# Kernel optimization log

Measured on AMD Instinct MI355X. Metric: run time of the kernel, lower is better.

## Reference

```python
import jax, jax.numpy as jnp
import numpy as np

B, S, D, E, H = 2, 1024, 1024, 16, 2048  # batch, seq, in_dim, num_experts, hidden_dim
TOP_K = 2
TEMP = 1.0


def setup_inputs() -> dict:
    key = jax.random.key(0)
    ks = jax.random.split(key, 4)
    sc_d = 1.0 / np.sqrt(D)
    sc_h = 1.0 / np.sqrt(H)
    return {
        "x": jax.random.normal(ks[0], (B, S, D), dtype=jnp.float32),
        "Wr": jax.random.normal(ks[1], (D, E), dtype=jnp.float32) * sc_d,  # router
        "br": jnp.zeros((E,), dtype=jnp.float32),
        "W1": jax.random.normal(ks[2], (E, D, H), dtype=jnp.float32) * sc_d,  # expert fc1
        "b1": jnp.zeros((E, H), dtype=jnp.float32),
        "W2": jax.random.normal(ks[3], (E, H, D), dtype=jnp.float32) * sc_h,  # expert fc2
        "b2": jnp.zeros((E, D), dtype=jnp.float32),
    }


def reference(x, Wr, br, W1, b1, W2, b2):
    token_shape = x.shape[:-1]
    d = x.shape[-1]
    xt = x.reshape(-1, d)  # [T, D] flattened tokens
    T = xt.shape[0]

    # Router: logits / temperature -> softmax -> top-k
    logits = (xt @ Wr + br) / TEMP
    probs = jax.nn.softmax(logits, axis=-1)          # [T, E]
    w, idx = jax.lax.top_k(probs, TOP_K)             # [T, K]
    w = w / jnp.clip(jnp.sum(w, axis=-1, keepdims=True), 1e-9)

    # Combine weights per (token, expert); top-k indices are unique per row
    comb = jnp.zeros((T, E), dtype=xt.dtype)
    comb = comb.at[jnp.arange(T)[:, None], idx].add(w)  # [T, E]

    # Per-expert 2-layer MLP with exact (erf) GELU, matching torch nn.GELU
    h = jax.nn.gelu(jnp.einsum('td,edh->teh', xt, W1) + b1, approximate=False)  # [T, E, H]
    o = jnp.einsum('teh,eho->teo', h, W2) + b2                                   # [T, E, D]
    y = jnp.einsum('teo,te->to', o, comb)                                        # [T, D]

    # residual (in_dim == out_dim)
    y = xt + y
    return y.reshape(*token_shape, d)
```

## Files before the change

kernel.cpp:

```cpp
#include <hip/hip_runtime.h>
#include <hip/hip_bf16.h>

#define T_TOK 2048
#define DIM   1024
#define NEXP  16
#define HID   2048
#define MAXMT 48

typedef __attribute__((ext_vector_type(8))) short short8;
typedef __attribute__((ext_vector_type(4))) float f32x4;

__device__ __forceinline__ unsigned short f2bf(float f) {
  __hip_bfloat16 h = __float2bfloat16(f);
  union { __hip_bfloat16 b; unsigned short u; } cv; cv.b = h; return cv.u;
}

__global__ void init_k(int* cnt, int* fill) {
  int i = threadIdx.x;
  if (i < NEXP) { cnt[i] = 0; fill[i] = 0; }
}

__global__ __launch_bounds__(256) void router_k(const float* __restrict__ x,
    const float* __restrict__ Wr, const float* __restrict__ br,
    int* __restrict__ re, float* __restrict__ rwv, int* __restrict__ cnt)
{
  const int wid = threadIdx.x >> 6, lane = threadIdx.x & 63;
  const int t = blockIdx.x * 4 + wid;
  const float* xr = x + (size_t)t * DIM;
  float acc[NEXP];
#pragma unroll
  for (int e = 0; e < NEXP; e++) acc[e] = 0.f;
  for (int i = 0; i < DIM / 64; i++) {
    const int d = lane + 64 * i;
    const float xv = xr[d];
    const float4* w4 = reinterpret_cast<const float4*>(Wr + (size_t)d * NEXP);
#pragma unroll
    for (int q = 0; q < 4; q++) {
      float4 w = w4[q];
      acc[4*q+0] += xv * w.x; acc[4*q+1] += xv * w.y;
      acc[4*q+2] += xv * w.z; acc[4*q+3] += xv * w.w;
    }
  }
#pragma unroll
  for (int e = 0; e < NEXP; e++) {
    float v = acc[e];
    v += __shfl_xor(v, 32); v += __shfl_xor(v, 16); v += __shfl_xor(v, 8);
    v += __shfl_xor(v, 4);  v += __shfl_xor(v, 2);  v += __shfl_xor(v, 1);
    acc[e] = v;
  }
  if (lane == 0) {
    float lg[NEXP];
#pragma unroll
    for (int e = 0; e < NEXP; e++) lg[e] = acc[e] + br[e];
    int e0 = 0; float b0 = lg[0];
    for (int e = 1; e < NEXP; e++) if (lg[e] > b0) { b0 = lg[e]; e0 = e; }
    int e1 = (e0 == 0) ? 1 : 0; float b1v = lg[e1];
    for (int e = 0; e < NEXP; e++) if (e != e0 && lg[e] > b1v) { b1v = lg[e]; e1 = e; }
    float p1 = expf(b1v - b0);
    float inv = 1.0f / (1.0f + p1);
    re[2*t] = e0; re[2*t+1] = e1;
    rwv[2*t] = inv; rwv[2*t+1] = p1 * inv;
    atomicAdd(&cnt[e0], 1); atomicAdd(&cnt[e1], 1);
  }
}

__global__ void scan_k(const int* cnt, int* basev, int* tile_e, int* tile_m0, int* ntt) {
  if (threadIdx.x == 0) {
    int s = 0, t = 0;
    for (int e = 0; e < NEXP; e++) {
      basev[e] = s;
      for (int m0 = 0; m0 < cnt[e]; m0 += 128) { tile_e[t] = e; tile_m0[t] = m0; t++; }
      s += cnt[e];
    }
    ntt[0] = t;
  }
}

__global__ __launch_bounds__(256) void scatter_k(const int* __restrict__ re,
    const float* __restrict__ rwv, const int* __restrict__ basev, int* fill,
    int* __restrict__ rows_token, float* __restrict__ rows_w, int* __restrict__ slot_of)
{
  int t = blockIdx.x * 256 + threadIdx.x;
  if (t >= T_TOK) return;
  for (int k = 0; k < 2; k++) {
    int e = re[2*t+k];
    int pos = atomicAdd(&fill[e], 1);
    int row = basev[e] + pos;
    rows_token[row] = t;
    rows_w[row] = rwv[2*t+k];
    slot_of[2*t+k] = row;
  }
}

__global__ __launch_bounds__(256) void gather_k(const float* __restrict__ x,
    const int* __restrict__ rows_token, unsigned short* __restrict__ xg)
{
  const int row = blockIdx.x, t = threadIdx.x;
  const int tok = rows_token[row];
  float4 v = reinterpret_cast<const float4*>(x + (size_t)tok * DIM)[t];
  ushort4 h;
  h.x = f2bf(v.x); h.y = f2bf(v.y); h.z = f2bf(v.z); h.w = f2bf(v.w);
  reinterpret_cast<ushort4*>(xg + (size_t)row * DIM)[t] = h;
}

template<bool FC1>
__global__ __launch_bounds__(256, 2) void expert_gemm_k(
    const unsigned short* __restrict__ Ag,
    const float* __restrict__ Wg, const float* __restrict__ bg,
    const int* __restrict__ cnt, const int* __restrict__ basev,
    const int* __restrict__ tile_e, const int* __restrict__ tile_m0,
    const int* __restrict__ ntt, const float* __restrict__ rows_w,
    unsigned short* __restrict__ hout, float* __restrict__ obuf)
{
  constexpr int KD = FC1 ? DIM : HID;
  constexpr int ND = FC1 ? HID : DIM;
  constexpr int KSPL = FC1 ? 1 : 2;
  constexpr int KLOC = KD / KSPL;
  constexpr int BM = 128, BN = 128, BK = 64;
  constexpr int NPH = KLOC / BK;
  if ((int)blockIdx.y >= ntt[0]) return;
  const int e  = tile_e[blockIdx.y], m0 = tile_m0[blockIdx.y];
  const int Ne = cnt[e], base = basev[e];
  const int nt = blockIdx.x;
  const int kz = blockIdx.z;
  const int kbase = kz * KLOC;
  __shared__ unsigned short As[BM][72];
  __shared__ unsigned short Bs[BN][72];
  const int tid = threadIdx.x;
  const float* W = Wg + (size_t)e * KD * ND + (size_t)kbase * ND + nt * BN;

  const unsigned short* aptr[4];
#pragma unroll
  for (int i = 0; i < 4; i++) {
    int g = m0 + (tid >> 3) + 32 * i; if (g >= Ne) g = Ne - 1;
    aptr[i] = Ag + (size_t)(base + g) * KD + kbase + (tid & 7) * 8;
  }
  const float* bbase = W + (size_t)((tid >> 7) * 4) * ND + (tid & 127);

  const int wid = tid >> 6, lane = tid & 63;
  const int wr = wid >> 1, wc = wid & 1;
  const int lr = lane & 15, lg = lane >> 4;
  const bool wactive = (m0 + wr * 64) < Ne;

  f32x4 acc[4][4];
#pragma unroll
  for (int m = 0; m < 4; m++)
#pragma unroll
    for (int n = 0; n < 4; n++) acc[m][n] = (f32x4){0.f, 0.f, 0.f, 0.f};

#define LOAD_SET(VA, VB, K0)                                                 \
  { _Pragma("unroll")                                                        \
    for (int i = 0; i < 4; i++)                                              \
      VA[i] = *reinterpret_cast<const short8*>(aptr[i] + (K0));              \
    _Pragma("unroll")                                                        \
    for (int i = 0; i < 8; i++) {                                            \
      const float* p = bbase + (size_t)((K0) + 8 * i) * ND;                  \
      VB[i].x = p[0]; VB[i].y = p[(size_t)ND];                               \
      VB[i].z = p[2 * (size_t)ND]; VB[i].w = p[3 * (size_t)ND];              \
    } }

#define STORE_SET(VA, VB)                                                    \
  { _Pragma("unroll")                                                        \
    for (int i = 0; i < 4; i++)                                              \
      *reinterpret_cast<short8*>(&As[(tid >> 3) + 32 * i][(tid & 7) * 8]) = VA[i]; \
    _Pragma("unroll")                                                        \
    for (int i = 0; i < 8; i++) {                                            \
      ushort4 h;                                                             \
      h.x = f2bf(VB[i].x); h.y = f2bf(VB[i].y);                              \
      h.z = f2bf(VB[i].z); h.w = f2bf(VB[i].w);                              \
      *reinterpret_cast<ushort4*>(&Bs[tid & 127][((tid >> 7) + 2 * i) * 4]) = h; \
    } }

#define MFMA_HALF(H)                                                         \
  if (wactive) {                                                             \
    short8 af[4], bb[4];                                                     \
    _Pragma("unroll")                                                        \
    for (int m = 0; m < 4; m++)                                              \
      af[m] = *reinterpret_cast<const short8*>(&As[wr*64 + m*16 + lr][(H)*32 + lg*8]); \
    _Pragma("unroll")                                                        \
    for (int n = 0; n < 4; n++)                                              \
      bb[n] = *reinterpret_cast<const short8*>(&Bs[wc*64 + n*16 + lr][(H)*32 + lg*8]); \
    _Pragma("unroll")                                                        \
    for (int m = 0; m < 4; m++)                                              \
      _Pragma("unroll")                                                      \
      for (int n = 0; n < 4; n++)                                            \
        acc[m][n] = __builtin_amdgcn_mfma_f32_16x16x32_bf16(af[m], bb[n],    \
                                                            acc[m][n], 0,0,0);\
  }

#define PHASE(VA, VB, PH)                                                    \
  STORE_SET(VA, VB)                                                          \
  __syncthreads();                                                           \
  if ((PH) + 2 < NPH) { LOAD_SET(VA, VB, ((PH) + 2) * BK) }                  \
  __builtin_amdgcn_s_setprio(1);                                             \
  MFMA_HALF(0)                                                               \
  MFMA_HALF(1)                                                               \
  __builtin_amdgcn_s_setprio(0);                                             \
  __syncthreads();

  short8 vaP[4], vaQ[4];
  float4 vbP[8], vbQ[8];
  LOAD_SET(vaP, vbP, 0)
  LOAD_SET(vaQ, vbQ, BK)

  for (int ph = 0; ph < NPH; ph += 2) {
    PHASE(vaP, vbP, ph)
    PHASE(vaQ, vbQ, ph + 1)
  }
#undef LOAD_SET
#undef STORE_SET
#undef MFMA_HALF
#undef PHASE

  if (!wactive) return;
#pragma unroll
  for (int n = 0; n < 4; n++) {
    const int col = nt * BN + wc * 64 + n * 16 + lr;
    const float bias = (kz == 0) ? bg[(size_t)e * ND + col] : 0.f;
#pragma unroll
    for (int m = 0; m < 4; m++) {
      const int rbase = m0 + wr * 64 + m * 16 + lg * 4;
#pragma unroll
      for (int v = 0; v < 4; v++) {
        const int r = rbase + v;
        if (r < Ne) {
          float val = acc[m][n][v] + bias;
          if constexpr (FC1) {
            val = 0.5f * val * (1.0f + erff(val * 0.70710678118654752440f));
            hout[(size_t)(base + r) * HID + col] = f2bf(val);
          } else {
            obuf[(size_t)kz * (2 * T_TOK) * DIM + (size_t)(base + r) * DIM + col]
                = val * rows_w[base + r];
          }
        }
      }
    }
  }
}

__global__ __launch_bounds__(256) void combine_k(const float* __restrict__ x,
    const float* __restrict__ obuf, const int* __restrict__ slot_of,
    float* __restrict__ out)
{
  const int t = blockIdx.x, c = threadIdx.x;
  const int s0 = slot_of[2*t], s1 = slot_of[2*t+1];
  const size_t PSZ = (size_t)(2 * T_TOK) * DIM;
  const float4 a  = reinterpret_cast<const float4*>(x + (size_t)t * DIM)[c];
  const float4 p0 = reinterpret_cast<const float4*>(obuf + (size_t)s0 * DIM)[c];
  const float4 p1 = reinterpret_cast<const float4*>(obuf + PSZ + (size_t)s0 * DIM)[c];
  const float4 q0 = reinterpret_cast<const float4*>(obuf + (size_t)s1 * DIM)[c];
  const float4 q1 = reinterpret_cast<const float4*>(obuf + PSZ + (size_t)s1 * DIM)[c];
  float4 r;
  r.x = a.x + p0.x + p1.x + q0.x + q1.x;
  r.y = a.y + p0.y + p1.y + q0.y + q1.y;
  r.z = a.z + p0.z + p1.z + q0.z + q1.z;
  r.w = a.w + p0.w + p1.w + q0.w + q1.w;
  reinterpret_cast<float4*>(out + (size_t)t * DIM)[c] = r;
}

extern "C" void kernel_launch(void* const* d_in, const int* in_sizes, int n_in,
                              void* d_out, int out_size, void* d_ws, size_t ws_size,
                              hipStream_t stream) {
  const float* x  = (const float*)d_in[0];
  const float* Wr = (const float*)d_in[1];
  const float* br = (const float*)d_in[2];
  const float* W1 = (const float*)d_in[3];
  const float* b1 = (const float*)d_in[4];
  const float* W2 = (const float*)d_in[5];
  const float* b2 = (const float*)d_in[6];
  float* out = (float*)d_out;
  char* ws = (char*)d_ws;

  int*   cnt        = (int*)  (ws + 0);
  int*   fill       = (int*)  (ws + 64);
  int*   basev      = (int*)  (ws + 128);
  int*   ntt        = (int*)  (ws + 192);
  int*   tile_e     = (int*)  (ws + 1024);
  int*   tile_m0    = (int*)  (ws + 2048);
  int*   re         = (int*)  (ws + 16384);
  float* rwv        = (float*)(ws + 32768);
  int*   rows_token = (int*)  (ws + 49152);
  float* rows_w     = (float*)(ws + 65536);
  int*   slot_of    = (int*)  (ws + 81920);
  unsigned short* xg   = (unsigned short*)(ws + ((size_t)(1 << 17)));
  unsigned short* hbuf = (unsigned short*)(ws + ((size_t)(1 << 17) + ((size_t)8 << 20)));
  float* obuf          = (float*)         (ws + ((size_t)(1 << 17) + ((size_t)24 << 20)));

  init_k<<<dim3(1), dim3(64), 0, stream>>>(cnt, fill);
  router_k<<<dim3(T_TOK / 4), dim3(256), 0, stream>>>(x, Wr, br, re, rwv, cnt);
  scan_k<<<dim3(1), dim3(64), 0, stream>>>(cnt, basev, tile_e, tile_m0, ntt);
  scatter_k<<<dim3(T_TOK / 256), dim3(256), 0, stream>>>(re, rwv, basev, fill,
                                                         rows_token, rows_w, slot_of);
  gather_k<<<dim3(2 * T_TOK), dim3(256), 0, stream>>>(x, rows_token, xg);
  expert_gemm_k<true><<<dim3(HID / 128, MAXMT, 1), dim3(256), 0, stream>>>(
      xg, W1, b1, cnt, basev, tile_e, tile_m0, ntt, rows_w, hbuf, obuf);
  expert_gemm_k<false><<<dim3(DIM / 128, MAXMT, 2), dim3(256), 0, stream>>>(
      hbuf, W2, b2, cnt, basev, tile_e, tile_m0, ntt, rows_w, hbuf, obuf);
  combine_k<<<dim3(T_TOK), dim3(256), 0, stream>>>(x, obuf, slot_of, out);
}
```

Measured before the change: 263.9 us.

## Pretranspose expert weights to bf16 and load tiles directly into LDS

Adds a per-call kernel that converts W1/W2 to bf16 in a K-contiguous transposed layout. The expert GEMM then loads A and B tiles with global_load_lds into XOR-swizzled shared memory and raises the occupancy hint. This removes the strided fp32 weight loads and in-loop conversions, halving the bytes the GEMMs read for weights. In exchange, the full fp32 weights are read and bf16 copies written on every call, and the register prefetch pipelining is dropped.

Measured after the change: 275.5 us. +4.4%, slower.

```diff
diff --git a/kernel.cpp b/kernel.cpp
--- a/kernel.cpp
+++ b/kernel.cpp
@@ -13,6 +13,12 @@
 __device__ __forceinline__ unsigned short f2bf(float f) {
   __hip_bfloat16 h = __float2bfloat16(f);
   union { __hip_bfloat16 b; unsigned short u; } cv; cv.b = h; return cv.u;
+}
+
+__device__ __forceinline__ void glds16(const void* g, void* l) {
+  __builtin_amdgcn_global_load_lds(
+      (const __attribute__((address_space(1))) unsigned int*)g,
+      (__attribute__((address_space(3))) unsigned int*)l, 16, 0, 0);
 }
 
 __global__ void init_k(int* cnt, int* fill) {
@@ -103,10 +109,40 @@
   reinterpret_cast<ushort4*>(xg + (size_t)row * DIM)[t] = h;
 }
 
+template<int KDIM, int NDIM>
+__global__ __launch_bounds__(256) void wtr_k(const float* __restrict__ W,
+                                             unsigned short* __restrict__ Wt)
+{
+  const int e = blockIdx.z;
+  const int k0 = blockIdx.y * 64, n0 = blockIdx.x * 64;
+  __shared__ unsigned short Ts[64][68];
+  const int t = threadIdx.x;
+  const int rr = t >> 4, cc = t & 15;
+#pragma unroll
+  for (int i = 0; i < 4; i++) {
+    const int kk = rr + 16 * i;
+    float4 v = *reinterpret_cast<const float4*>(
+        W + ((size_t)e * KDIM + k0 + kk) * NDIM + n0 + cc * 4);
+    Ts[kk][cc*4+0] = f2bf(v.x); Ts[kk][cc*4+1] = f2bf(v.y);
+    Ts[kk][cc*4+2] = f2bf(v.z); Ts[kk][cc*4+3] = f2bf(v.w);
+  }
+  __syncthreads();
+#pragma unroll
+  for (int i = 0; i < 4; i++) {
+    const int nn = rr + 16 * i;
+    ushort4 o;
+    o.x = Ts[cc*4+0][nn]; o.y = Ts[cc*4+1][nn];
+    o.z = Ts[cc*4+2][nn]; o.w = Ts[cc*4+3][nn];
+    *reinterpret_cast<ushort4*>(
+        Wt + ((size_t)e * NDIM + n0 + nn) * KDIM + k0 + cc * 4) = o;
+  }
+}
+
 template<bool FC1>
-__global__ __launch_bounds__(256, 2) void expert_gemm_k(
+__global__ __launch_bounds__(256, 3) void expert_gemm_k(
     const unsigned short* __restrict__ Ag,
-    const float* __restrict__ Wg, const float* __restrict__ bg,
+    const unsigned short* __restrict__ Wt,
+    const float* __restrict__ bg,
     const int* __restrict__ cnt, const int* __restrict__ basev,
     const int* __restrict__ tile_e, const int* __restrict__ tile_m0,
     const int* __restrict__ ntt, const float* __restrict__ rows_w,
@@ -121,96 +157,78 @@
   if ((int)blockIdx.y >= ntt[0]) return;
   const int e  = tile_e[blockIdx.y], m0 = tile_m0[blockIdx.y];
   const int Ne = cnt[e], base = basev[e];
-  const int nt = blockIdx.x;
-  const int kz = blockIdx.z;
+  const int nt = blockIdx.x, kz = blockIdx.z;
   const int kbase = kz * KLOC;
-  __shared__ unsigned short As[BM][72];
-  __shared__ unsigned short Bs[BN][72];
-  const int tid = threadIdx.x;
-  const float* W = Wg + (size_t)e * KD * ND + (size_t)kbase * ND + nt * BN;
-
-  const unsigned short* aptr[4];
-#pragma unroll
-  for (int i = 0; i < 4; i++) {
-    int g = m0 + (tid >> 3) + 32 * i; if (g >= Ne) g = Ne - 1;
-    aptr[i] = Ag + (size_t)(base + g) * KD + kbase + (tid & 7) * 8;
-  }
-  const float* bbase = W + (size_t)((tid >> 7) * 4) * ND + (tid & 127);
-
-  const int wid = tid >> 6, lane = tid & 63;
+  __shared__ unsigned short As[BM][BK];
+  __shared__ unsigned short Bs[BN][BK];
+  const int tid = threadIdx.x, lane = tid & 63, wid = tid >> 6;
+
+  const int lrow = lane >> 3;
+  const int lchunk = ((lane & 7) ^ (lrow & 7)) * 8;
+  const unsigned short* asrc[4];
+  const unsigned short* bsrc[4];
+  unsigned short* aldst[4];
+  unsigned short* bldst[4];
+#pragma unroll
+  for (int j = 0; j < 4; j++) {
+    const int r = j * 32 + wid * 8 + lrow;
+    int g = m0 + r; if (g >= Ne) g = Ne - 1;
+    asrc[j] = Ag + (size_t)(base + g) * KD + kbase + lchunk;
+    aldst[j] = &As[j * 32 + wid * 8][0];
+    bsrc[j] = Wt + ((size_t)e * ND + nt * BN + r) * KD + kbase + lchunk;
+    bldst[j] = &Bs[j * 32 + wid * 8][0];
+  }
+
   const int wr = wid >> 1, wc = wid & 1;
   const int lr = lane & 15, lg = lane >> 4;
   const bool wactive = (m0 + wr * 64) < Ne;
 
+  const unsigned short* afp[4][2];
+  const unsigned short* bfp[4][2];
+#pragma unroll
+  for (int m = 0; m < 4; m++)
+#pragma unroll
+    for (int h = 0; h < 2; h++) {
+      afp[m][h] = &As[wr * 64 + m * 16 + lr][(((lg + 4*h) ^ (lr & 7)) * 8)];
+      bfp[m][h] = &Bs[wc * 64 + m * 16 + lr][(((lg + 4*h) ^ (lr & 7)) * 8)];
+    }
+
   f32x4 acc[4][4];
 #pragma unroll
   for (int m = 0; m < 4; m++)
 #pragma unroll
     for (int n = 0; n < 4; n++) acc[m][n] = (f32x4){0.f, 0.f, 0.f, 0.f};
 
-#define LOAD_SET(VA, VB, K0)                                                 \
-  { _Pragma("unroll")                                                        \
-    for (int i = 0; i < 4; i++)                                              \
-      VA[i] = *reinterpret_cast<const short8*>(aptr[i] + (K0));              \
-    _Pragma("unroll")                                                        \
-    for (int i = 0; i < 8; i++) {                                            \
-      const float* p = bbase + (size_t)((K0) + 8 * i) * ND;                  \
-      VB[i].x = p[0]; VB[i].y = p[(size_t)ND];                               \
-      VB[i].z = p[2 * (size_t)ND]; VB[i].w = p[3 * (size_t)ND];              \
-    } }
-
-#define STORE_SET(VA, VB)                                                    \
-  { _Pragma("unroll")                                                        \
-    for (int i = 0; i < 4; i++)                                              \
-      *reinterpret_cast<short8*>(&As[(tid >> 3) + 32 * i][(tid & 7) * 8]) = VA[i]; \
-    _Pragma("unroll")                                                        \
-    for (int i = 0; i < 8; i++) {                                            \
-      ushort4 h;                                                             \
-      h.x = f2bf(VB[i].x); h.y = f2bf(VB[i].y);                              \
-      h.z = f2bf(VB[i].z); h.w = f2bf(VB[i].w);                              \
-      *reinterpret_cast<ushort4*>(&Bs[tid & 127][((tid >> 7) + 2 * i) * 4]) = h; \
-    } }
-
-#define MFMA_HALF(H)                                                         \
-  if (wactive) {                                                             \
-    short8 af[4], bb[4];                                                     \
-    _Pragma("unroll")                                                        \
-    for (int m = 0; m < 4; m++)                                              \
-      af[m] = *reinterpret_cast<const short8*>(&As[wr*64 + m*16 + lr][(H)*32 + lg*8]); \
-    _Pragma("unroll")                                                        \
-    for (int n = 0; n < 4; n++)                                              \
-      bb[n] = *reinterpret_cast<const short8*>(&Bs[wc*64 + n*16 + lr][(H)*32 + lg*8]); \
-    _Pragma("unroll")                                                        \
-    for (int m = 0; m < 4; m++)                                              \
-      _Pragma("unroll")                                                      \
-      for (int n = 0; n < 4; n++)                                            \
-        acc[m][n] = __builtin_amdgcn_mfma_f32_16x16x32_bf16(af[m], bb[n],    \
-                                                            acc[m][n], 0,0,0);\
-  }
-
-#define PHASE(VA, VB, PH)                                                    \
-  STORE_SET(VA, VB)                                                          \
-  __syncthreads();                                                           \
-  if ((PH) + 2 < NPH) { LOAD_SET(VA, VB, ((PH) + 2) * BK) }                  \
-  __builtin_amdgcn_s_setprio(1);                                             \
-  MFMA_HALF(0)                                                               \
-  MFMA_HALF(1)                                                               \
-  __builtin_amdgcn_s_setprio(0);                                             \
-  __syncthreads();
-
-  short8 vaP[4], vaQ[4];
-  float4 vbP[8], vbQ[8];
-  LOAD_SET(vaP, vbP, 0)
-  LOAD_SET(vaQ, vbQ, BK)
-
-  for (int ph = 0; ph < NPH; ph += 2) {
-    PHASE(vaP, vbP, ph)
-    PHASE(vaQ, vbQ, ph + 1)
-  }
-#undef LOAD_SET
-#undef STORE_SET
-#undef MFMA_HALF
-#undef PHASE
+  for (int ph = 0; ph < NPH; ++ph) {
+    const int k0 = ph * BK;
+    __syncthreads();
+#pragma unroll
+    for (int j = 0; j < 4; j++) {
+      glds16(asrc[j] + k0, aldst[j]);
+      glds16(bsrc[j] + k0, bldst[j]);
+    }
+    __syncthreads();
+    if (wactive) {
+      __builtin_amdgcn_s_setprio(1);
+#pragma unroll
+      for (int h = 0; h < 2; h++) {
+        short8 af[4], bb[4];
+#pragma unroll
+        for (int m = 0; m < 4; m++)
+          af[m] = *reinterpret_cast<const short8*>(afp[m][h]);
+#pragma unroll
+        for (int n = 0; n < 4; n++)
+          bb[n] = *reinterpret_cast<const short8*>(bfp[n][h]);
+#pragma unroll
+        for (int m = 0; m < 4; m++)
+#pragma unroll
+          for (int n = 0; n < 4; n++)
+            acc[m][n] = __builtin_amdgcn_mfma_f32_16x16x32_bf16(af[m], bb[n],
+                                                                acc[m][n], 0, 0, 0);
+      }
+      __builtin_amdgcn_s_setprio(0);
+    }
+  }
 
   if (!wactive) return;
 #pragma unroll
@@ -283,8 +301,10 @@
   float* rows_w     = (float*)(ws + 65536);
   int*   slot_of    = (int*)  (ws + 81920);
   unsigned short* xg   = (unsigned short*)(ws + ((size_t)(1 << 17)));
-  unsigned short* hbuf = (unsigned short*)(ws + ((size_t)(1 << 17) + ((size_t)8 << 20)));
-  float* obuf          = (float*)         (ws + ((size_t)(1 << 17) + ((size_t)24 << 20)));
+  unsigned short* hbuf = (unsigned short*)(ws + ((size_t)(1 << 17) + ((size_t)8  << 20)));
+  float*          obuf = (float*)         (ws + ((size_t)(1 << 17) + ((size_t)24 << 20)));
+  unsigned short* W1t  = (unsigned short*)(ws + ((size_t)(1 << 17) + ((size_t)56 << 20)));
+  unsigned short* W2t  = (unsigned short*)(ws + ((size_t)(1 << 17) + ((size_t)120 << 20)));
 
   init_k<<<dim3(1), dim3(64), 0, stream>>>(cnt, fill);
   router_k<<<dim3(T_TOK / 4), dim3(256), 0, stream>>>(x, Wr, br, re, rwv, cnt);
@@ -292,9 +312,11 @@
   scatter_k<<<dim3(T_TOK / 256), dim3(256), 0, stream>>>(re, rwv, basev, fill,
                                                          rows_token, rows_w, slot_of);
   gather_k<<<dim3(2 * T_TOK), dim3(256), 0, stream>>>(x, rows_token, xg);
+  wtr_k<DIM, HID><<<dim3(HID / 64, DIM / 64, NEXP), dim3(256), 0, stream>>>(W1, W1t);
+  wtr_k<HID, DIM><<<dim3(DIM / 64, HID / 64, NEXP), dim3(256), 0, stream>>>(W2, W2t);
   expert_gemm_k<true><<<dim3(HID / 128, MAXMT, 1), dim3(256), 0, stream>>>(
-      xg, W1, b1, cnt, basev, tile_e, tile_m0, ntt, rows_w, hbuf, obuf);
+      xg, W1t, b1, cnt, basev, tile_e, tile_m0, ntt, rows_w, hbuf, obuf);
   expert_gemm_k<false><<<dim3(DIM / 128, MAXMT, 2), dim3(256), 0, stream>>>(
-      hbuf, W2, b2, cnt, basev, tile_e, tile_m0, ntt, rows_w, hbuf, obuf);
+      hbuf, W2t, b2, cnt, basev, tile_e, tile_m0, ntt, rows_w, hbuf, obuf);
   combine_k<<<dim3(T_TOK), dim3(256), 0, stream>>>(x, obuf, slot_of, out);
 }
```
